# Performance work log

Measured on AMD Instinct MI355X. Metric: run time of the kernel, lower is better.

The kernel has to match this reference:

```python
import jax, jax.numpy as jnp
import numpy as np
import math

EMBED_DIM = 1024
NUM_HEADS = 16
HEAD_DIM = EMBED_DIM // NUM_HEADS
MAX_LEN = 5000
LN_EPS = 1e-5


def _positional_encoding(max_len, embed_dim):
    pos = np.arange(max_len, dtype=np.float32)[:, None]
    div = np.exp(np.arange(0, embed_dim, 2, dtype=np.float32) * (-math.log(10000.0) / embed_dim))
    pe = np.zeros((max_len, embed_dim), dtype=np.float32)
    pe[:, 0::2] = np.sin(pos * div)
    pe[:, 1::2] = np.cos(pos * div)
    return jnp.asarray(pe)[None]  # [1, max_len, D]


def setup_inputs() -> dict:
    key = jax.random.key(0)
    ks = jax.random.split(key, 12)
    s = 1.0 / math.sqrt(EMBED_DIM)
    D = EMBED_DIM
    return {
        "x": jax.random.normal(ks[0], (4, 2048, D), dtype=jnp.float32),
        "wq": jax.random.uniform(ks[1], (D, D), jnp.float32, -s, s),
        "bq": jax.random.uniform(ks[2], (D,), jnp.float32, -s, s),
        "wk": jax.random.uniform(ks[3], (D, D), jnp.float32, -s, s),
        "bk": jax.random.uniform(ks[4], (D,), jnp.float32, -s, s),
        "wv": jax.random.uniform(ks[5], (D, D), jnp.float32, -s, s),
        "bv": jax.random.uniform(ks[6], (D,), jnp.float32, -s, s),
        "wo": jax.random.uniform(ks[7], (D, D), jnp.float32, -s, s),
        "bo": jax.random.uniform(ks[8], (D,), jnp.float32, -s, s),
        "gamma": jnp.ones((D,), jnp.float32),
        "beta": jnp.zeros((D,), jnp.float32),
        "pe": _positional_encoding(MAX_LEN, D),
    }


def reference(x, wq, bq, wk, bk, wv, bv, wo, bo, gamma, beta, pe):
    B, S, D = x.shape
    H, Hd = NUM_HEADS, HEAD_DIM
    x = x + pe[:, :S, :]
    # projections; weights stored as [in, out]
    q = (x @ wq + bq).reshape(B, S, H, Hd).transpose(0, 2, 1, 3)
    k = (x @ wk + bk).reshape(B, S, H, Hd).transpose(0, 2, 1, 3)
    v = (x @ wv + bv).reshape(B, S, H, Hd).transpose(0, 2, 1, 3)
    scores = jnp.einsum("bhqd,bhkd->bhqk", q, k) / math.sqrt(Hd)
    attn = jax.nn.softmax(scores, axis=-1)  # dropout is identity in eval
    out = jnp.einsum("bhqk,bhkd->bhqd", attn, v)
    out = out.transpose(0, 2, 1, 3).reshape(B, S, D)
    out = out @ wo + bo
    # residual + layernorm
    h = out + x
    mu = jnp.mean(h, axis=-1, keepdims=True)
    var = jnp.var(h, axis=-1, keepdims=True)
    return (h - mu) * jax.lax.rsqrt(var + LN_EPS) * gamma + beta
```

## Files before the change

kernel.cpp:

```cpp
#include <hip/hip_runtime.h>

#define DEV __device__ __forceinline__

typedef __attribute__((ext_vector_type(4))) float floatx4;
typedef __attribute__((ext_vector_type(8))) short short8;

DEV unsigned short f2bf(float f) {
  unsigned u = __float_as_uint(f);
  u += 0x7FFF + ((u >> 16) & 1);
  return (unsigned short)(u >> 16);
}
DEV float bf2f(unsigned short h) { return __uint_as_float(((unsigned)h) << 16); }

DEV unsigned pkbf(float lo, float hi) {
  return __builtin_amdgcn_perm(__float_as_uint(hi) + 0x8000u,
                               __float_as_uint(lo) + 0x8000u, 0x07060302u);
}

#if __has_builtin(__builtin_amdgcn_exp2f)
#define EXP2(x) __builtin_amdgcn_exp2f(x)
#else
#define EXP2(x) exp2f(x)
#endif

#define GLD16(g, l)                                                            \
  __builtin_amdgcn_global_load_lds(                                            \
      (const __attribute__((address_space(1))) void*)(g),                      \
      (__attribute__((address_space(3))) void*)(l), 16, 0, 0)

__global__ void k_wt(const float* __restrict__ w0, const float* __restrict__ w1,
                     const float* __restrict__ w2, const float* __restrict__ w3,
                     unsigned short* __restrict__ wt) {
  __shared__ float t[64][65];
  const float* wsel = (blockIdx.z == 0) ? w0
                    : (blockIdx.z == 1) ? w1
                    : (blockIdx.z == 2) ? w2 : w3;
  unsigned short* out = wt + (size_t)blockIdx.z * 1024 * 1024;
  const int tx = threadIdx.x, ty = threadIdx.y;
  const int k0 = blockIdx.x * 64, n0 = blockIdx.y * 64;
  for (int i = ty; i < 64; i += 4)
    t[i][tx] = wsel[(size_t)(k0 + i) * 1024 + n0 + tx];
  __syncthreads();
  for (int i = ty; i < 64; i += 4)
    out[(size_t)(n0 + i) * 1024 + k0 + tx] = f2bf(t[tx][i]);
}

__global__ void k_addpe(const float* __restrict__ x, const float* __restrict__ pe,
                        float* __restrict__ xf, unsigned short* __restrict__ xb) {
  const int idx = blockIdx.x * 256 + threadIdx.x;
  const int row = idx >> 8;
  const int c4 = idx & 255;
  const int s = row & 2047;
  const float4 xv = ((const float4*)x)[idx];
  const float4 pv = ((const float4*)pe)[s * 256 + c4];
  float4 r;
  r.x = xv.x + pv.x; r.y = xv.y + pv.y; r.z = xv.z + pv.z; r.w = xv.w + pv.w;
  ((float4*)xf)[idx] = r;
  ushort4 o;
  o.x = f2bf(r.x); o.y = f2bf(r.y); o.z = f2bf(r.z); o.w = f2bf(r.w);
  ((ushort4*)xb)[idx] = o;
}

__global__ __launch_bounds__(256) void k_gemmqk(
    const unsigned short* __restrict__ A, const unsigned short* __restrict__ Bt,
    const float* __restrict__ bqp, const float* __restrict__ bkp,
    unsigned short* __restrict__ qb, unsigned short* __restrict__ kb) {
  __shared__ unsigned short As[128 * 32];
  __shared__ unsigned short Bs[128 * 32];
  const int tid = threadIdx.x;
  const int lane = tid & 63, wave = tid >> 6;
  const int quad = lane >> 4, l16 = lane & 15;
  const int wm = wave >> 1, wn = wave & 1;
  const int rb = blockIdx.x * 128, cb = blockIdx.y * 128;
  const int which = cb >> 10;
  const float* bias = (which == 0) ? bqp : bkp;
  unsigned short* out = (which == 0) ? qb : kb;

  floatx4 acc[4][4];
  const floatx4 vzero = {0.f, 0.f, 0.f, 0.f};
#pragma unroll
  for (int i = 0; i < 4; ++i)
#pragma unroll
    for (int j = 0; j < 4; ++j) acc[i][j] = vzero;

  for (int k0 = 0; k0 < 1024; k0 += 32) {
#pragma unroll
    for (int r = 0; r < 2; ++r) {
      const int c = r * 256 + tid;
      const int arow = c >> 2, koff = (c & 3) << 3;
      GLD16(A + (size_t)(rb + arow) * 1024 + k0 + koff,
            As + (size_t)(r * 256 + wave * 64) * 8);
      GLD16(Bt + (size_t)(cb + arow) * 1024 + k0 + koff,
            Bs + (size_t)(r * 256 + wave * 64) * 8);
    }
    __syncthreads();
    short8 fa[4], fb[4];
#pragma unroll
    for (int i = 0; i < 4; ++i) {
      fa[i] = *(const short8*)(As + (wm * 64 + i * 16 + l16) * 32 + quad * 8);
      fb[i] = *(const short8*)(Bs + (wn * 64 + i * 16 + l16) * 32 + quad * 8);
    }
#pragma unroll
    for (int mi = 0; mi < 4; ++mi)
#pragma unroll
      for (int ni = 0; ni < 4; ++ni)
        acc[mi][ni] =
            __builtin_amdgcn_mfma_f32_16x16x32_bf16(fa[mi], fb[ni], acc[mi][ni], 0, 0, 0);
    __syncthreads();
  }

#pragma unroll
  for (int ni = 0; ni < 4; ++ni) {
    const int col = cb + wn * 64 + ni * 16 + l16;
    const int cl = col & 1023;
    const float bvv = bias[cl];
    const int h = cl >> 6, d = cl & 63;
#pragma unroll
    for (int mi = 0; mi < 4; ++mi) {
#pragma unroll
      for (int r = 0; r < 4; ++r) {
        const int row = rb + wm * 64 + mi * 16 + quad * 4 + r;
        const int b = row >> 11, s = row & 2047;
        out[((size_t)(b * 16 + h) * 2048 + s) * 64 + d] = f2bf(acc[mi][ni][r] + bvv);
      }
    }
  }
}

__global__ __launch_bounds__(256) void k_gemmvt(
    const unsigned short* __restrict__ Av, const unsigned short* __restrict__ Bx,
    const float* __restrict__ bias, unsigned short* __restrict__ out) {
  __shared__ unsigned short As[128 * 32];
  __shared__ unsigned short Bs[128 * 32];
  const int tid = threadIdx.x;
  const int lane = tid & 63, wave = tid >> 6;
  const int quad = lane >> 4, l16 = lane & 15;
  const int wm = wave >> 1, wn = wave & 1;
  const int rb = blockIdx.x * 128, cb = blockIdx.y * 128;

  floatx4 acc[4][4];
  const floatx4 vzero = {0.f, 0.f, 0.f, 0.f};
#pragma unroll
  for (int i = 0; i < 4; ++i)
#pragma unroll
    for (int j = 0; j < 4; ++j) acc[i][j] = vzero;

  for (int k0 = 0; k0 < 1024; k0 += 32) {
#pragma unroll
    for (int r = 0; r < 2; ++r) {
      const int c = r * 256 + tid;
      const int arow = c >> 2, koff = (c & 3) << 3;
      GLD16(Av + (size_t)(rb + arow) * 1024 + k0 + koff,
            As + (size_t)(r * 256 + wave * 64) * 8);
      GLD16(Bx + (size_t)(cb + arow) * 1024 + k0 + koff,
            Bs + (size_t)(r * 256 + wave * 64) * 8);
    }
    __syncthreads();
    short8 fa[4], fb[4];
#pragma unroll
    for (int i = 0; i < 4; ++i) {
      fa[i] = *(const short8*)(As + (wm * 64 + i * 16 + l16) * 32 + quad * 8);
      fb[i] = *(const short8*)(Bs + (wn * 64 + i * 16 + l16) * 32 + quad * 8);
    }
#pragma unroll
    for (int mi = 0; mi < 4; ++mi)
#pragma unroll
      for (int ni = 0; ni < 4; ++ni)
        acc[mi][ni] =
            __builtin_amdgcn_mfma_f32_16x16x32_bf16(fa[mi], fb[ni], acc[mi][ni], 0, 0, 0);
    __syncthreads();
  }

#pragma unroll
  for (int mi = 0; mi < 4; ++mi) {
#pragma unroll
    for (int r = 0; r < 4; ++r) {
      const int row = rb + wm * 64 + mi * 16 + quad * 4 + r;
      const float bvv = bias[row];
#pragma unroll
      for (int ni = 0; ni < 4; ++ni) {
        const int col = cb + wn * 64 + ni * 16 + l16;
        out[((size_t)(col >> 11) * 1024 + row) * 2048 + (col & 2047)] =
            f2bf(acc[mi][ni][r] + bvv);
      }
    }
  }
}

__global__ __launch_bounds__(256) void k_gemmo(
    const unsigned short* __restrict__ A, const unsigned short* __restrict__ Bt,
    const float* __restrict__ bias, unsigned short* __restrict__ out) {
  __shared__ unsigned short As[128 * 32];
  __shared__ unsigned short Bs[128 * 32];
  const int tid = threadIdx.x;
  const int lane = tid & 63, wave = tid >> 6;
  const int quad = lane >> 4, l16 = lane & 15;
  const int wm = wave >> 1, wn = wave & 1;
  const int rb = blockIdx.x * 128, cb = blockIdx.y * 128;

  floatx4 acc[4][4];
  const floatx4 vzero = {0.f, 0.f, 0.f, 0.f};
#pragma unroll
  for (int i = 0; i < 4; ++i)
#pragma unroll
    for (int j = 0; j < 4; ++j) acc[i][j] = vzero;

  for (int k0 = 0; k0 < 1024; k0 += 32) {
#pragma unroll
    for (int r = 0; r < 2; ++r) {
      const int c = r * 256 + tid;
      const int arow = c >> 2, koff = (c & 3) << 3;
      GLD16(A + (size_t)(rb + arow) * 1024 + k0 + koff,
            As + (size_t)(r * 256 + wave * 64) * 8);
      GLD16(Bt + (size_t)(cb + arow) * 1024 + k0 + koff,
            Bs + (size_t)(r * 256 + wave * 64) * 8);
    }
    __syncthreads();
    short8 fa[4], fb[4];
#pragma unroll
    for (int i = 0; i < 4; ++i) {
      fa[i] = *(const short8*)(As + (wm * 64 + i * 16 + l16) * 32 + quad * 8);
      fb[i] = *(const short8*)(Bs + (wn * 64 + i * 16 + l16) * 32 + quad * 8);
    }
#pragma unroll
    for (int mi = 0; mi < 4; ++mi)
#pragma unroll
      for (int ni = 0; ni < 4; ++ni)
        acc[mi][ni] =
            __builtin_amdgcn_mfma_f32_16x16x32_bf16(fa[mi], fb[ni], acc[mi][ni], 0, 0, 0);
    __syncthreads();
  }

#pragma unroll
  for (int ni = 0; ni < 4; ++ni) {
    const int col = cb + wn * 64 + ni * 16 + l16;
    const float bvv = bias[col];
#pragma unroll
    for (int mi = 0; mi < 4; ++mi) {
#pragma unroll
      for (int r = 0; r < 4; ++r) {
        const int row = rb + wm * 64 + mi * 16 + quad * 4 + r;
        out[(size_t)row * 1024 + col] = f2bf(acc[mi][ni][r] + bvv);
      }
    }
  }
}

__global__ __launch_bounds__(256, 4) void k_flash(
    const unsigned short* __restrict__ Q, const unsigned short* __restrict__ Kb,
    const unsigned short* __restrict__ Vt, unsigned short* __restrict__ AO) {
  __shared__ unsigned short Ks[64 * 64];
  __shared__ unsigned short Vs[64 * 64];
  __shared__ unsigned short Ps[4][32 * 72];
  const int tid = threadIdx.x, lane = tid & 63, wave = tid >> 6;
  const int quad = lane >> 4, l16 = lane & 15;
  const int g = blockIdx.x;
  const int li = g >> 3;
  const int bh = (g & 7) * 8 + (li >> 4);
  const int qt = li & 15;
  const int b = bh >> 4, h = bh & 15;

  const unsigned short* Kh = Kb + (size_t)bh * 2048 * 64;
  const unsigned short* Vh = Vt + (size_t)bh * 64 * 2048;

  const float LAMBDA = 0.125f * 1.4426950408889634f;
  short8 aq[2][2];
  {
    const unsigned short* Qb = Q + ((size_t)bh * 2048 + qt * 128 + wave * 32) * 64;
#pragma unroll
    for (int qi = 0; qi < 2; ++qi)
#pragma unroll
      for (int c = 0; c < 2; ++c) {
        const short8 raw =
            *(const short8*)(Qb + (size_t)(qi * 16 + l16) * 64 + c * 32 + quad * 8);
        short8 sv;
#pragma unroll
        for (int j = 0; j < 8; ++j)
          sv[j] = (short)f2bf(bf2f((unsigned short)raw[j]) * LAMBDA);
        aq[qi][c] = sv;
      }
  }

  short8 onesv;
#pragma unroll
  for (int j = 0; j < 8; ++j) onesv[j] = (short)0x3F80;

  const floatx4 vzero = {0.f, 0.f, 0.f, 0.f};
  floatx4 o[2][4];
#pragma unroll
  for (int qi = 0; qi < 2; ++qi)
#pragma unroll
    for (int di = 0; di < 4; ++di) o[qi][di] = vzero;
  floatx4 lacc[2] = {vzero, vzero};
  unsigned short* Pw = Ps[wave];

#define STAGE(ktile)                                                           \
  {                                                                            \
    _Pragma("unroll") for (int r = 0; r < 2; ++r) {                            \
      const int c = r * 256 + tid;                                             \
      const int rw = c >> 3;                                                   \
      const int gc = ((c & 7) ^ (rw & 7)) * 8;                                 \
      GLD16(Kh + (size_t)((ktile) * 64 + rw) * 64 + gc,                        \
            &Ks[(size_t)(r * 256 + wave * 64) * 8]);                           \
      GLD16(Vh + (size_t)rw * 2048 + (ktile) * 64 + gc,                        \
            &Vs[(size_t)(r * 256 + wave * 64) * 8]);                           \
    }                                                                          \
  }

  STAGE(0);
  __syncthreads();

  for (int kt = 0; kt < 32; ++kt) {
    short8 fk[4][2];
#pragma unroll
    for (int ni = 0; ni < 4; ++ni)
#pragma unroll
      for (int c = 0; c < 2; ++c)
        fk[ni][c] = *(const short8*)(&Ks[(ni * 16 + l16) * 64 +
                                         (((c * 4 + quad) ^ (l16 & 7)) << 3)]);

#pragma unroll
    for (int qi = 0; qi < 2; ++qi) {
      floatx4 p[4];
#pragma unroll
      for (int ni = 0; ni < 4; ++ni) {
        floatx4 t = vzero;
#pragma unroll
        for (int c = 0; c < 2; ++c)
          t = __builtin_amdgcn_mfma_f32_16x16x32_bf16(fk[ni][c], aq[qi][c], t, 0, 0, 0);
        p[ni] = t;
      }
#pragma unroll
      for (int ni = 0; ni < 4; ++ni)
#pragma unroll
        for (int r = 0; r < 4; ++r) p[ni][r] = EXP2(p[ni][r]);
#pragma unroll
      for (int ni = 0; ni < 4; ++ni) {
        uint2 pk;
        pk.x = pkbf(p[ni][0], p[ni][1]);
        pk.y = pkbf(p[ni][2], p[ni][3]);
        *(uint2*)(&Pw[(qi * 16 + l16) * 72 + ni * 16 + quad * 4]) = pk;
      }
    }
    asm volatile("s_waitcnt lgkmcnt(0)" ::: "memory");

#pragma unroll
    for (int c = 0; c < 2; ++c) {
      short8 ap[2];
#pragma unroll
      for (int qi = 0; qi < 2; ++qi)
        ap[qi] = *(const short8*)(&Pw[(qi * 16 + l16) * 72 + c * 32 + quad * 8]);
#pragma unroll
      for (int qi = 0; qi < 2; ++qi)
        lacc[qi] = __builtin_amdgcn_mfma_f32_16x16x32_bf16(ap[qi], onesv, lacc[qi], 0, 0, 0);
#pragma unroll
      for (int di = 0; di < 4; ++di) {
        const short8 fv = *(const short8*)(&Vs[(di * 16 + l16) * 64 +
                                               (((c * 4 + quad) ^ (l16 & 7)) << 3)]);
#pragma unroll
        for (int qi = 0; qi < 2; ++qi)
          o[qi][di] = __builtin_amdgcn_mfma_f32_16x16x32_bf16(ap[qi], fv, o[qi][di], 0, 0, 0);
      }
    }
    __syncthreads();
    if (kt + 1 < 32) STAGE(kt + 1);
    __syncthreads();
  }

#pragma unroll
  for (int qi = 0; qi < 2; ++qi) {
    float invl[4];
#pragma unroll
    for (int r = 0; r < 4; ++r) invl[r] = __builtin_amdgcn_rcpf(lacc[qi][r]);
#pragma unroll
    for (int di = 0; di < 4; ++di) {
#pragma unroll
      for (int r = 0; r < 4; ++r) {
        const int s = qt * 128 + wave * 32 + qi * 16 + quad * 4 + r;
        const int col = h * 64 + di * 16 + l16;
        AO[((size_t)b * 2048 + s) * 1024 + col] = f2bf(o[qi][di][r] * invl[r]);
      }
    }
  }
#undef STAGE
}

__global__ __launch_bounds__(256) void k_ln(
    const unsigned short* __restrict__ proj, const float* __restrict__ xpe,
    const float* __restrict__ gamma, const float* __restrict__ beta,
    float* __restrict__ out) {
  const int row = blockIdx.x, tid = threadIdx.x;
  const int lane = tid & 63, wave = tid >> 6;
  const float4 xv = ((const float4*)(xpe + (size_t)row * 1024))[tid];
  const ushort4 pv = ((const ushort4*)(proj + (size_t)row * 1024))[tid];
  const float h0 = xv.x + bf2f(pv.x);
  const float h1 = xv.y + bf2f(pv.y);
  const float h2 = xv.z + bf2f(pv.z);
  const float h3 = xv.w + bf2f(pv.w);
  float s = h0 + h1 + h2 + h3;
  float s2 = h0 * h0 + h1 * h1 + h2 * h2 + h3 * h3;
#pragma unroll
  for (int m = 1; m < 64; m <<= 1) {
    s += __shfl_xor(s, m);
    s2 += __shfl_xor(s2, m);
  }
  __shared__ float rs[4], rq[4];
  if (lane == 0) { rs[wave] = s; rq[wave] = s2; }
  __syncthreads();
  s = rs[0] + rs[1] + rs[2] + rs[3];
  s2 = rq[0] + rq[1] + rq[2] + rq[3];
  const float mu = s * (1.f / 1024.f);
  const float var = s2 * (1.f / 1024.f) - mu * mu;
  const float rstd = rsqrtf(var + 1e-5f);
  const float4 gv = ((const float4*)gamma)[tid];
  const float4 bvv = ((const float4*)beta)[tid];
  float4 ov;
  ov.x = (h0 - mu) * rstd * gv.x + bvv.x;
  ov.y = (h1 - mu) * rstd * gv.y + bvv.y;
  ov.z = (h2 - mu) * rstd * gv.z + bvv.z;
  ov.w = (h3 - mu) * rstd * gv.w + bvv.w;
  ((float4*)(out + (size_t)row * 1024))[tid] = ov;
}

extern "C" void kernel_launch(void* const* d_in, const int* in_sizes, int n_in,
                              void* d_out, int out_size, void* d_ws, size_t ws_size,
                              hipStream_t stream) {
  const float* x = (const float*)d_in[0];
  const float* wq = (const float*)d_in[1];
  const float* bq = (const float*)d_in[2];
  const float* wk = (const float*)d_in[3];
  const float* bk = (const float*)d_in[4];
  const float* wv = (const float*)d_in[5];
  const float* bv = (const float*)d_in[6];
  const float* wo = (const float*)d_in[7];
  const float* bo = (const float*)d_in[8];
  const float* gamma = (const float*)d_in[9];
  const float* beta = (const float*)d_in[10];
  const float* pe = (const float*)d_in[11];

  if (ws_size < 125829120) return;

  char* w = (char*)d_ws;
  unsigned short* wt = (unsigned short*)(w);
  float* xpef = (float*)(w + 8388608);
  unsigned short* xpeb = (unsigned short*)(w + 41943040);
  unsigned short* qb = (unsigned short*)(w + 58720256);
  unsigned short* kb = (unsigned short*)(w + 75497472);
  unsigned short* vtb = (unsigned short*)(w + 92274688);
  unsigned short* aob = (unsigned short*)(w + 109051904);
  unsigned short* projb = qb;

  k_wt<<<dim3(16, 16, 4), dim3(64, 4), 0, stream>>>(wq, wk, wv, wo, wt);
  k_addpe<<<8192, 256, 0, stream>>>(x, pe, xpef, xpeb);
  k_gemmqk<<<dim3(64, 16), 256, 0, stream>>>(xpeb, wt, bq, bk, qb, kb);
  k_gemmvt<<<dim3(8, 64), 256, 0, stream>>>(wt + 2097152, xpeb, bv, vtb);
  k_flash<<<1024, 256, 0, stream>>>(qb, kb, vtb, aob);
  k_gemmo<<<dim3(64, 8), 256, 0, stream>>>(aob, wt + 3145728, bo, projb);
  k_ln<<<8192, 256, 0, stream>>>(projb, xpef, gamma, beta, (float*)d_out);
}
```

Before: 334.7 us.

## Merge prep and QKV GEMM launches, widen K tile with XOR-swizzled LDS

Merges the weight-transpose and add-PE kernels into one launch, and the QK and V^T projection GEMMs into one 1536-block launch, which removes launch gaps. The GEMM core moves from a K tile of 32 to 64 and uses an XOR-swizzled LDS layout so the fragment reads avoid bank conflicts. Block IDs are remapped so tiles that share operands land on the same XCD, improving L2 reuse. Doubling the LDS footprint together with launch_bounds(256,4) may lower occupancy or raise register pressure.

```diff
diff --git a/kernel.cpp b/kernel.cpp
--- a/kernel.cpp
+++ b/kernel.cpp
@@ -28,53 +28,81 @@
       (const __attribute__((address_space(1))) void*)(g),                      \
       (__attribute__((address_space(3))) void*)(l), 16, 0, 0)
 
-__global__ void k_wt(const float* __restrict__ w0, const float* __restrict__ w1,
-                     const float* __restrict__ w2, const float* __restrict__ w3,
-                     unsigned short* __restrict__ wt) {
+__global__ void k_prep(const float* __restrict__ x, const float* __restrict__ pe,
+                       const float* __restrict__ w0, const float* __restrict__ w1,
+                       const float* __restrict__ w2, const float* __restrict__ w3,
+                       unsigned short* __restrict__ wt, float* __restrict__ xf,
+                       unsigned short* __restrict__ xb) {
   __shared__ float t[64][65];
-  const float* wsel = (blockIdx.z == 0) ? w0
-                    : (blockIdx.z == 1) ? w1
-                    : (blockIdx.z == 2) ? w2 : w3;
-  unsigned short* out = wt + (size_t)blockIdx.z * 1024 * 1024;
-  const int tx = threadIdx.x, ty = threadIdx.y;
-  const int k0 = blockIdx.x * 64, n0 = blockIdx.y * 64;
-  for (int i = ty; i < 64; i += 4)
-    t[i][tx] = wsel[(size_t)(k0 + i) * 1024 + n0 + tx];
-  __syncthreads();
-  for (int i = ty; i < 64; i += 4)
-    out[(size_t)(n0 + i) * 1024 + k0 + tx] = f2bf(t[tx][i]);
-}
-
-__global__ void k_addpe(const float* __restrict__ x, const float* __restrict__ pe,
-                        float* __restrict__ xf, unsigned short* __restrict__ xb) {
-  const int idx = blockIdx.x * 256 + threadIdx.x;
-  const int row = idx >> 8;
-  const int c4 = idx & 255;
-  const int s = row & 2047;
-  const float4 xv = ((const float4*)x)[idx];
-  const float4 pv = ((const float4*)pe)[s * 256 + c4];
-  float4 r;
-  r.x = xv.x + pv.x; r.y = xv.y + pv.y; r.z = xv.z + pv.z; r.w = xv.w + pv.w;
-  ((float4*)xf)[idx] = r;
-  ushort4 o;
-  o.x = f2bf(r.x); o.y = f2bf(r.y); o.z = f2bf(r.z); o.w = f2bf(r.w);
-  ((ushort4*)xb)[idx] = o;
-}
-
-__global__ __launch_bounds__(256) void k_gemmqk(
-    const unsigned short* __restrict__ A, const unsigned short* __restrict__ Bt,
+  const int bid = blockIdx.x, tid = threadIdx.x;
+  if (bid < 1024) {
+    const int z = bid >> 8, rem = bid & 255;
+    const int bx = rem & 15, by = rem >> 4;
+    const int tx = tid & 63, ty = tid >> 6;
+    const float* wsel = (z == 0) ? w0 : (z == 1) ? w1 : (z == 2) ? w2 : w3;
+    unsigned short* out = wt + (size_t)z * 1048576;
+    const int k0 = bx * 64, n0 = by * 64;
+    for (int i = ty; i < 64; i += 4)
+      t[i][tx] = wsel[(size_t)(k0 + i) * 1024 + n0 + tx];
+    __syncthreads();
+    for (int i = ty; i < 64; i += 4)
+      out[(size_t)(n0 + i) * 1024 + k0 + tx] = f2bf(t[tx][i]);
+  } else {
+    const int idx = (bid - 1024) * 256 + tid;
+    const int row = idx >> 8;
+    const int c4 = idx & 255;
+    const int s = row & 2047;
+    const float4 xv = ((const float4*)x)[idx];
+    const float4 pv = ((const float4*)pe)[s * 256 + c4];
+    float4 r;
+    r.x = xv.x + pv.x; r.y = xv.y + pv.y; r.z = xv.z + pv.z; r.w = xv.w + pv.w;
+    ((float4*)xf)[idx] = r;
+    ushort4 o;
+    o.x = f2bf(r.x); o.y = f2bf(r.y); o.z = f2bf(r.z); o.w = f2bf(r.w);
+    ((ushort4*)xb)[idx] = o;
+  }
+}
+
+#define GEMM_CORE(Aptr, Bptr, RB, CB)                                          \
+  for (int k0 = 0; k0 < 1024; k0 += 64) {                                      \
+    _Pragma("unroll") for (int r = 0; r < 4; ++r) {                            \
+      const int c = r * 256 + tid;                                             \
+      const int rw = c >> 3;                                                   \
+      const int gc = ((c & 7) ^ (rw & 7)) << 3;                                \
+      GLD16((Aptr) + (size_t)((RB) + rw) * 1024 + k0 + gc,                     \
+            As + (size_t)(r * 256 + wave * 64) * 8);                           \
+      GLD16((Bptr) + (size_t)((CB) + rw) * 1024 + k0 + gc,                     \
+            Bs + (size_t)(r * 256 + wave * 64) * 8);                           \
+    }                                                                          \
+    __syncthreads();                                                           \
+    _Pragma("unroll") for (int kk = 0; kk < 2; ++kk) {                         \
+      short8 fa[4], fb[4];                                                     \
+      _Pragma("unroll") for (int i = 0; i < 4; ++i) {                          \
+        fa[i] = *(const short8*)(As + (wm * 64 + i * 16 + l16) * 64 +          \
+                                 (((kk * 4 + quad) ^ (l16 & 7)) << 3));        \
+        fb[i] = *(const short8*)(Bs + (wn * 64 + i * 16 + l16) * 64 +          \
+                                 (((kk * 4 + quad) ^ (l16 & 7)) << 3));        \
+      }                                                                        \
+      _Pragma("unroll") for (int mi = 0; mi < 4; ++mi)                         \
+          _Pragma("unroll") for (int ni = 0; ni < 4; ++ni) acc[mi][ni] =       \
+          __builtin_amdgcn_mfma_f32_16x16x32_bf16(fa[mi], fb[ni],              \
+                                                  acc[mi][ni], 0, 0, 0);       \
+    }                                                                          \
+    __syncthreads();                                                           \
+  }
+
+__global__ __launch_bounds__(256, 4) void k_gemmqkvt(
+    const unsigned short* __restrict__ xpeb, const unsigned short* __restrict__ wt,
     const float* __restrict__ bqp, const float* __restrict__ bkp,
-    unsigned short* __restrict__ qb, unsigned short* __restrict__ kb) {
-  __shared__ unsigned short As[128 * 32];
-  __shared__ unsigned short Bs[128 * 32];
+    const float* __restrict__ bvp, unsigned short* __restrict__ qb,
+    unsigned short* __restrict__ kb, unsigned short* __restrict__ vtb) {
+  __shared__ unsigned short As[128 * 64];
+  __shared__ unsigned short Bs[128 * 64];
   const int tid = threadIdx.x;
   const int lane = tid & 63, wave = tid >> 6;
   const int quad = lane >> 4, l16 = lane & 15;
   const int wm = wave >> 1, wn = wave & 1;
-  const int rb = blockIdx.x * 128, cb = blockIdx.y * 128;
-  const int which = cb >> 10;
-  const float* bias = (which == 0) ? bqp : bkp;
-  unsigned short* out = (which == 0) ? qb : kb;
+  const int id = blockIdx.x;
 
   floatx4 acc[4][4];
   const floatx4 vzero = {0.f, 0.f, 0.f, 0.f};
@@ -83,153 +111,75 @@
 #pragma unroll
     for (int j = 0; j < 4; ++j) acc[i][j] = vzero;
 
-  for (int k0 = 0; k0 < 1024; k0 += 32) {
-#pragma unroll
-    for (int r = 0; r < 2; ++r) {
-      const int c = r * 256 + tid;
-      const int arow = c >> 2, koff = (c & 3) << 3;
-      GLD16(A + (size_t)(rb + arow) * 1024 + k0 + koff,
-            As + (size_t)(r * 256 + wave * 64) * 8);
-      GLD16(Bt + (size_t)(cb + arow) * 1024 + k0 + koff,
-            Bs + (size_t)(r * 256 + wave * 64) * 8);
-    }
-    __syncthreads();
-    short8 fa[4], fb[4];
-#pragma unroll
-    for (int i = 0; i < 4; ++i) {
-      fa[i] = *(const short8*)(As + (wm * 64 + i * 16 + l16) * 32 + quad * 8);
-      fb[i] = *(const short8*)(Bs + (wn * 64 + i * 16 + l16) * 32 + quad * 8);
-    }
-#pragma unroll
-    for (int mi = 0; mi < 4; ++mi)
-#pragma unroll
-      for (int ni = 0; ni < 4; ++ni)
-        acc[mi][ni] =
-            __builtin_amdgcn_mfma_f32_16x16x32_bf16(fa[mi], fb[ni], acc[mi][ni], 0, 0, 0);
-    __syncthreads();
-  }
-
-#pragma unroll
-  for (int ni = 0; ni < 4; ++ni) {
-    const int col = cb + wn * 64 + ni * 16 + l16;
-    const int cl = col & 1023;
-    const float bvv = bias[cl];
-    const int h = cl >> 6, d = cl & 63;
+  if (id < 1024) {
+    const int xcd = id & 7, j = id >> 3;
+    const int bx = (xcd << 3) | (j & 7), by = j >> 3;
+    const int rb = bx * 128, cb = by * 128;
+    GEMM_CORE(xpeb, wt, rb, cb);
+    const int which = cb >> 10;
+    const float* bias = (which == 0) ? bqp : bkp;
+    unsigned short* out = (which == 0) ? qb : kb;
+#pragma unroll
+    for (int ni = 0; ni < 4; ++ni) {
+      const int col = cb + wn * 64 + ni * 16 + l16;
+      const int cl = col & 1023;
+      const float bvv = bias[cl];
+      const int h = cl >> 6, d = cl & 63;
+#pragma unroll
+      for (int mi = 0; mi < 4; ++mi) {
+#pragma unroll
+        for (int r = 0; r < 4; ++r) {
+          const int row = rb + wm * 64 + mi * 16 + quad * 4 + r;
+          const int b = row >> 11, s = row & 2047;
+          out[((size_t)(b * 16 + h) * 2048 + s) * 64 + d] = f2bf(acc[mi][ni][r] + bvv);
+        }
+      }
+    }
+  } else {
+    const int id2 = id - 1024;
+    const int xcd = id2 & 7, j = id2 >> 3;
+    const int by = (xcd << 3) | (j & 7), bx = j >> 3;
+    const int rb = bx * 128, cb = by * 128;
+    GEMM_CORE(wt + 2097152, xpeb, rb, cb);
 #pragma unroll
     for (int mi = 0; mi < 4; ++mi) {
 #pragma unroll
       for (int r = 0; r < 4; ++r) {
         const int row = rb + wm * 64 + mi * 16 + quad * 4 + r;
-        const int b = row >> 11, s = row & 2047;
-        out[((size_t)(b * 16 + h) * 2048 + s) * 64 + d] = f2bf(acc[mi][ni][r] + bvv);
-      }
-    }
-  }
-}
-
-__global__ __launch_bounds__(256) void k_gemmvt(
-    const unsigned short* __restrict__ Av, const unsigned short* __restrict__ Bx,
+        const float bvv = bvp[row];
+#pragma unroll
+        for (int ni = 0; ni < 4; ++ni) {
+          const int col = cb + wn * 64 + ni * 16 + l16;
+          vtb[((size_t)(col >> 11) * 1024 + row) * 2048 + (col & 2047)] =
+              f2bf(acc[mi][ni][r] + bvv);
+        }
+      }
+    }
+  }
+}
+
+__global__ __launch_bounds__(256, 4) void k_gemmo(
+    const unsigned short* __restrict__ A, const unsigned short* __restrict__ Bt,
     const float* __restrict__ bias, unsigned short* __restrict__ out) {
-  __shared__ unsigned short As[128 * 32];
-  __shared__ unsigned short Bs[128 * 32];
+  __shared__ unsigned short As[128 * 64];
+  __shared__ unsigned short Bs[128 * 64];
   const int tid = threadIdx.x;
   const int lane = tid & 63, wave = tid >> 6;
   const int quad = lane >> 4, l16 = lane & 15;
   const int wm = wave >> 1, wn = wave & 1;
-  const int rb = blockIdx.x * 128, cb = blockIdx.y * 128;
+  const int id = blockIdx.x;
+  const int xcd = id & 7, j = id >> 3;
+  const int bx = (xcd << 3) | (j & 7), by = j >> 3;
+  const int rb = bx * 128, cb = by * 128;
 
   floatx4 acc[4][4];
   const floatx4 vzero = {0.f, 0.f, 0.f, 0.f};
 #pragma unroll
   for (int i = 0; i < 4; ++i)
 #pragma unroll
-    for (int j = 0; j < 4; ++j) acc[i][j] = vzero;
-
-  for (int k0 = 0; k0 < 1024; k0 += 32) {
-#pragma unroll
-    for (int r = 0; r < 2; ++r) {
-      const int c = r * 256 + tid;
-      const int arow = c >> 2, koff = (c & 3) << 3;
-      GLD16(Av + (size_t)(rb + arow) * 1024 + k0 + koff,
-            As + (size_t)(r * 256 + wave * 64) * 8);
-      GLD16(Bx + (size_t)(cb + arow) * 1024 + k0 + koff,
-            Bs + (size_t)(r * 256 + wave * 64) * 8);
-    }
-    __syncthreads();
-    short8 fa[4], fb[4];
-#pragma unroll
-    for (int i = 0; i < 4; ++i) {
-      fa[i] = *(const short8*)(As + (wm * 64 + i * 16 + l16) * 32 + quad * 8);
-      fb[i] = *(const short8*)(Bs + (wn * 64 + i * 16 + l16) * 32 + quad * 8);
-    }
-#pragma unroll
-    for (int mi = 0; mi < 4; ++mi)
-#pragma unroll
-      for (int ni = 0; ni < 4; ++ni)
-        acc[mi][ni] =
-            __builtin_amdgcn_mfma_f32_16x16x32_bf16(fa[mi], fb[ni], acc[mi][ni], 0, 0, 0);
-    __syncthreads();
-  }
-
-#pragma unroll
-  for (int mi = 0; mi < 4; ++mi) {
-#pragma unroll
-    for (int r = 0; r < 4; ++r) {
-      const int row = rb + wm * 64 + mi * 16 + quad * 4 + r;
-      const float bvv = bias[row];
-#pragma unroll
-      for (int ni = 0; ni < 4; ++ni) {
-        const int col = cb + wn * 64 + ni * 16 + l16;
-        out[((size_t)(col >> 11) * 1024 + row) * 2048 + (col & 2047)] =
-            f2bf(acc[mi][ni][r] + bvv);
-      }
-    }
-  }
-}
-
-__global__ __launch_bounds__(256) void k_gemmo(
-    const unsigned short* __restrict__ A, const unsigned short* __restrict__ Bt,
-    const float* __restrict__ bias, unsigned short* __restrict__ out) {
-  __shared__ unsigned short As[128 * 32];
-  __shared__ unsigned short Bs[128 * 32];
-  const int tid = threadIdx.x;
-  const int lane = tid & 63, wave = tid >> 6;
-  const int quad = lane >> 4, l16 = lane & 15;
-  const int wm = wave >> 1, wn = wave & 1;
-  const int rb = blockIdx.x * 128, cb = blockIdx.y * 128;
-
-  floatx4 acc[4][4];
-  const floatx4 vzero = {0.f, 0.f, 0.f, 0.f};
-#pragma unroll
-  for (int i = 0; i < 4; ++i)
-#pragma unroll
-    for (int j = 0; j < 4; ++j) acc[i][j] = vzero;
-
-  for (int k0 = 0; k0 < 1024; k0 += 32) {
-#pragma unroll
-    for (int r = 0; r < 2; ++r) {
-      const int c = r * 256 + tid;
-      const int arow = c >> 2, koff = (c & 3) << 3;
-      GLD16(A + (size_t)(rb + arow) * 1024 + k0 + koff,
-            As + (size_t)(r * 256 + wave * 64) * 8);
-      GLD16(Bt + (size_t)(cb + arow) * 1024 + k0 + koff,
-            Bs + (size_t)(r * 256 + wave * 64) * 8);
-    }
-    __syncthreads();
-    short8 fa[4], fb[4];
-#pragma unroll
-    for (int i = 0; i < 4; ++i) {
-      fa[i] = *(const short8*)(As + (wm * 64 + i * 16 + l16) * 32 + quad * 8);
-      fb[i] = *(const short8*)(Bs + (wn * 64 + i * 16 + l16) * 32 + quad * 8);
-    }
-#pragma unroll
-    for (int mi = 0; mi < 4; ++mi)
-#pragma unroll
-      for (int ni = 0; ni < 4; ++ni)
-        acc[mi][ni] =
-            __builtin_amdgcn_mfma_f32_16x16x32_bf16(fa[mi], fb[ni], acc[mi][ni], 0, 0, 0);
-    __syncthreads();
-  }
+    for (int jj = 0; jj < 4; ++jj) acc[i][jj] = vzero;
+
+  GEMM_CORE(A, Bt, rb, cb);
 
 #pragma unroll
   for (int ni = 0; ni < 4; ++ni) {
@@ -450,11 +400,9 @@
   unsigned short* aob = (unsigned short*)(w + 109051904);
   unsigned short* projb = qb;
 
-  k_wt<<<dim3(16, 16, 4), dim3(64, 4), 0, stream>>>(wq, wk, wv, wo, wt);
-  k_addpe<<<8192, 256, 0, stream>>>(x, pe, xpef, xpeb);
-  k_gemmqk<<<dim3(64, 16), 256, 0, stream>>>(xpeb, wt, bq, bk, qb, kb);
-  k_gemmvt<<<dim3(8, 64), 256, 0, stream>>>(wt + 2097152, xpeb, bv, vtb);
+  k_prep<<<9216, 256, 0, stream>>>(x, pe, wq, wk, wv, wo, wt, xpef, xpeb);
+  k_gemmqkvt<<<1536, 256, 0, stream>>>(xpeb, wt, bq, bk, bv, qb, kb, vtb);
   k_flash<<<1024, 256, 0, stream>>>(qb, kb, vtb, aob);
-  k_gemmo<<<dim3(64, 8), 256, 0, stream>>>(aob, wt + 3145728, bo, projb);
+  k_gemmo<<<512, 256, 0, stream>>>(aob, wt + 3145728, bo, projb);
   k_ln<<<8192, 256, 0, stream>>>(projb, xpef, gamma, beta, (float*)d_out);
 }
```

Result: faster. 303.4 us (-9.3%).
